# Optimization experiments

Hardware: AMD Instinct MI355X
Metric: run time of the kernel (lower is better)

## Reference

```python
import jax, jax.numpy as jnp
import numpy as np

V_SIZE = 128000  # vocab size (v_size init arg)


def setup_inputs() -> dict:
    key = jax.random.key(0)
    k1, k2 = jax.random.split(key)
    # per-position scores -> weighting_scheme (softmax over seq dim)
    w_es = jax.random.normal(k1, (256, 2048), dtype=jnp.float32)
    # instance['x']: token ids in [0, v_size)
    x = jax.random.randint(k2, (256, 2048), 0, V_SIZE, dtype=jnp.int64)
    return {"w_es": w_es, "x": x}


def reference(w_es, x):
    # weighting_scheme(indices, w_es, instance): softmax over sequence positions
    weights = jax.nn.softmax(w_es, axis=-1)          # [B, S]
    B, S = weights.shape
    rows = jnp.arange(B)[:, None]                    # [B, 1] broadcast against [B, S]
    # scatter: w_a[b, x[b, i]] = weights[b, i]  (vectorized index_put)
    w_a = jnp.zeros((B, V_SIZE), dtype=weights.dtype).at[rows, x].set(weights)
    return (w_a, weights)
```

## Files before the change

### kernel.cpp

```cpp
#include <hip/hip_runtime.h>

#define BATCH 256
#define SEQ   2048
#define VOCAB 128000
#define HALF   64000
#define PCHUNK 16000
#define NPH    4

typedef float v4f __attribute__((ext_vector_type(4)));
typedef int   v4i __attribute__((ext_vector_type(4)));
typedef float v2f __attribute__((ext_vector_type(2)));
typedef int   v2i __attribute__((ext_vector_type(2)));

#define LBAR() do { asm volatile("s_waitcnt lgkmcnt(0)" ::: "memory"); \
                    __builtin_amdgcn_s_barrier(); } while (0)

__global__ __launch_bounds__(1024, 4)
void softmax_scatter_phased(const float* __restrict__ w_es,
                            const int*   __restrict__ x,
                            float* __restrict__ w_a,
                            float* __restrict__ w_out)
{
    __shared__ int   chunk[PCHUNK];
    __shared__ float red[32];

    const int bid = blockIdx.x;
    const int r = bid & (BATCH - 1);
    const int h = bid >> 8;
    const int base0 = h * HALF;

    const int t = threadIdx.x;
    const int lane = t & 63;
    const int wid  = t >> 6;

    {
        const v4i m1 = (v4i)(-1);
        #pragma unroll
        for (int j0 = 0; j0 < 4096; j0 += 1024) {
            const int j = j0 + t;
            if (j < (PCHUNK >> 2)) ((v4i*)chunk)[j] = m1;
        }
    }

    const float* rowp = w_es + (size_t)r * SEQ;
    const v2f a = ((const v2f*)rowp)[t];

    float m = fmaxf(a.x, a.y);
    #pragma unroll
    for (int off = 32; off > 0; off >>= 1)
        m = fmaxf(m, __shfl_down(m, off, 64));
    if (lane == 0) red[wid] = m;
    __syncthreads();
    m = red[0];
    #pragma unroll
    for (int k = 1; k < 16; ++k) m = fmaxf(m, red[k]);

    const float e0 = __expf(a.x - m);
    const float e1 = __expf(a.y - m);
    float s = e0 + e1;
    #pragma unroll
    for (int off = 32; off > 0; off >>= 1)
        s += __shfl_down(s, off, 64);
    if (lane == 0) red[16 + wid] = s;
    __syncthreads();
    s = red[16];
    #pragma unroll
    for (int k = 1; k < 16; ++k) s += red[16 + k];

    const float inv = 1.0f / s;
    const float w0 = e0 * inv;
    const float w1 = e1 * inv;

    if (h == 0) {
        v2f wv; wv.x = w0; wv.y = w1;
        ((v2f*)(w_out + (size_t)r * SEQ))[t] = wv;
    }

    const v2i xv = ((const v2i*)(x + (size_t)r * SEQ))[t];
    const int i0 = 2 * t;
    const int i1 = 2 * t + 1;

    float* const growp = w_a + (size_t)r * VOCAB;

    for (int p = 0; p < NPH; ++p) {
        const int pb = base0 + p * PCHUNK;
        const int v0 = xv.x - pb;
        const int v1 = xv.y - pb;
        const bool in0 = (unsigned)v0 < (unsigned)PCHUNK;
        const bool in1 = (unsigned)v1 < (unsigned)PCHUNK;

        if (in0) atomicMax(&chunk[v0], i0);
        if (in1) atomicMax(&chunk[v1], i1);
        LBAR();

        if (in0 && chunk[v0] == i0) ((float*)chunk)[v0] = w0;
        if (in1 && chunk[v1] == i1) ((float*)chunk)[v1] = w1;
        LBAR();

        float* gp = growp + pb;
        #pragma unroll
        for (int j0 = 0; j0 < 4096; j0 += 1024) {
            const int j = j0 + t;
            if (j < (PCHUNK >> 2)) {
                v4i b = ((const v4i*)chunk)[j];
                v4f o;
                o.x = (b.x < 0) ? 0.0f : __int_as_float(b.x);
                o.y = (b.y < 0) ? 0.0f : __int_as_float(b.y);
                o.z = (b.z < 0) ? 0.0f : __int_as_float(b.z);
                o.w = (b.w < 0) ? 0.0f : __int_as_float(b.w);
                ((v4f*)gp)[j] = o;
            }
        }

        if (p < NPH - 1) {
            LBAR();
            const v4i m1 = (v4i)(-1);
            #pragma unroll
            for (int j0 = 0; j0 < 4096; j0 += 1024) {
                const int j = j0 + t;
                if (j < (PCHUNK >> 2)) ((v4i*)chunk)[j] = m1;
            }
            LBAR();
        }
    }
}

extern "C" void kernel_launch(void* const* d_in, const int* in_sizes, int n_in,
                              void* d_out, int out_size, void* d_ws, size_t ws_size,
                              hipStream_t stream) {
    const float* w_es = (const float*)d_in[0];
    const int*   x    = (const int*)d_in[1];

    float* out  = (float*)d_out;
    float* w_a  = out;
    float* w    = out + (size_t)BATCH * VOCAB;

    softmax_scatter_phased<<<2 * BATCH, 1024, 0, stream>>>(w_es, x, w_a, w);
}
```

Baseline: 136.6 us.

## Replace phased LDS chunk scatter with LDS hash table plus occupancy bitmap

Each block now inserts its in-range token ids into a 4096-slot open-addressing hash table in shared memory. The table resolves duplicate ids by atomicMax on the position, then swaps in the winning softmax weight. A bitmap marks occupied vocab entries, so the block writes its whole 64000-entry half of the output row in one pass, probing the hash only for set bits. This removes the four-phase loop with its repeated chunk clears and barriers, and shrinks LDS use, which may raise occupancy. In exchange it adds CAS-based linear probing and hash lookups during the write-out.

```diff
diff --git a/kernel.cpp b/kernel.cpp
--- a/kernel.cpp
+++ b/kernel.cpp
@@ -3,9 +3,8 @@
 #define BATCH 256
 #define SEQ   2048
 #define VOCAB 128000
-#define HALF   64000
-#define PCHUNK 16000
-#define NPH    4
+#define HALF  64000
+#define HSLOT 4096
 
 typedef float v4f __attribute__((ext_vector_type(4)));
 typedef int   v4i __attribute__((ext_vector_type(4)));
@@ -15,35 +14,37 @@
 #define LBAR() do { asm volatile("s_waitcnt lgkmcnt(0)" ::: "memory"); \
                     __builtin_amdgcn_s_barrier(); } while (0)
 
+__device__ __forceinline__ int hash_v(int v) {
+    return (int)(((unsigned)v * 2654435761u) >> 20);
+}
+
 __global__ __launch_bounds__(1024, 4)
-void softmax_scatter_phased(const float* __restrict__ w_es,
-                            const int*   __restrict__ x,
-                            float* __restrict__ w_a,
-                            float* __restrict__ w_out)
+void softmax_scatter_hash(const float* __restrict__ w_es,
+                          const int*   __restrict__ x,
+                          float* __restrict__ w_a,
+                          float* __restrict__ w_out)
 {
-    __shared__ int   chunk[PCHUNK];
-    __shared__ float red[32];
+    __shared__ int      key[HSLOT];
+    __shared__ int      val[HSLOT];
+    __shared__ unsigned bm[HALF / 32];
+    __shared__ float    red[32];
 
     const int bid = blockIdx.x;
     const int r = bid & (BATCH - 1);
     const int h = bid >> 8;
-    const int base0 = h * HALF;
-
     const int t = threadIdx.x;
     const int lane = t & 63;
     const int wid  = t >> 6;
 
     {
         const v4i m1 = (v4i)(-1);
-        #pragma unroll
-        for (int j0 = 0; j0 < 4096; j0 += 1024) {
-            const int j = j0 + t;
-            if (j < (PCHUNK >> 2)) ((v4i*)chunk)[j] = m1;
-        }
+        ((v4i*)key)[t] = m1;
+        ((v4i*)val)[t] = m1;
+        if (t < (HALF / 32 / 4)) ((v4i*)bm)[t] = (v4i)(0);
     }
 
-    const float* rowp = w_es + (size_t)r * SEQ;
-    const v2f a = ((const v2f*)rowp)[t];
+    const v2f a  = ((const v2f*)(w_es + (size_t)r * SEQ))[t];
+    const v2i xv = ((const v2i*)(x    + (size_t)r * SEQ))[t];
 
     float m = fmaxf(a.x, a.y);
     #pragma unroll
@@ -54,6 +55,34 @@
     m = red[0];
     #pragma unroll
     for (int k = 1; k < 16; ++k) m = fmaxf(m, red[k]);
+
+    const int i0 = 2 * t;
+    const int i1 = 2 * t + 1;
+    const int v0 = xv.x - h * HALF;
+    const int v1 = xv.y - h * HALF;
+    const bool in0 = (unsigned)v0 < (unsigned)HALF;
+    const bool in1 = (unsigned)v1 < (unsigned)HALF;
+
+    if (in0) {
+        atomicOr(&bm[v0 >> 5], 1u << (v0 & 31));
+        int s = hash_v(v0);
+        while (true) {
+            int k = atomicCAS(&key[s], -1, v0);
+            if (k == -1 || k == v0) break;
+            s = (s + 1) & (HSLOT - 1);
+        }
+        atomicMax(&val[s], i0);
+    }
+    if (in1) {
+        atomicOr(&bm[v1 >> 5], 1u << (v1 & 31));
+        int s = hash_v(v1);
+        while (true) {
+            int k = atomicCAS(&key[s], -1, v1);
+            if (k == -1 || k == v1) break;
+            s = (s + 1) & (HSLOT - 1);
+        }
+        atomicMax(&val[s], i1);
+    }
 
     const float e0 = __expf(a.x - m);
     const float e1 = __expf(a.y - m);
@@ -76,52 +105,35 @@
         ((v2f*)(w_out + (size_t)r * SEQ))[t] = wv;
     }
 
-    const v2i xv = ((const v2i*)(x + (size_t)r * SEQ))[t];
-    const int i0 = 2 * t;
-    const int i1 = 2 * t + 1;
+    if (in0) {
+        int sl = hash_v(v0);
+        while (key[sl] != v0) sl = (sl + 1) & (HSLOT - 1);
+        if (val[sl] == i0) val[sl] = __float_as_int(w0);
+    }
+    if (in1) {
+        int sl = hash_v(v1);
+        while (key[sl] != v1) sl = (sl + 1) & (HSLOT - 1);
+        if (val[sl] == i1) val[sl] = __float_as_int(w1);
+    }
+    LBAR();
 
-    float* const growp = w_a + (size_t)r * VOCAB;
-
-    for (int p = 0; p < NPH; ++p) {
-        const int pb = base0 + p * PCHUNK;
-        const int v0 = xv.x - pb;
-        const int v1 = xv.y - pb;
-        const bool in0 = (unsigned)v0 < (unsigned)PCHUNK;
-        const bool in1 = (unsigned)v1 < (unsigned)PCHUNK;
-
-        if (in0) atomicMax(&chunk[v0], i0);
-        if (in1) atomicMax(&chunk[v1], i1);
-        LBAR();
-
-        if (in0 && chunk[v0] == i0) ((float*)chunk)[v0] = w0;
-        if (in1 && chunk[v1] == i1) ((float*)chunk)[v1] = w1;
-        LBAR();
-
-        float* gp = growp + pb;
-        #pragma unroll
-        for (int j0 = 0; j0 < 4096; j0 += 1024) {
-            const int j = j0 + t;
-            if (j < (PCHUNK >> 2)) {
-                v4i b = ((const v4i*)chunk)[j];
-                v4f o;
-                o.x = (b.x < 0) ? 0.0f : __int_as_float(b.x);
-                o.y = (b.y < 0) ? 0.0f : __int_as_float(b.y);
-                o.z = (b.z < 0) ? 0.0f : __int_as_float(b.z);
-                o.w = (b.w < 0) ? 0.0f : __int_as_float(b.w);
-                ((v4f*)gp)[j] = o;
+    float* gp = w_a + (size_t)r * VOCAB + h * HALF;
+    for (int g = t; g < (HALF >> 2); g += 1024) {
+        const unsigned word = bm[g >> 3];
+        const unsigned nib  = (word >> ((g & 7) << 2)) & 0xFu;
+        v4f o = (v4f)(0.0f);
+        if (nib) {
+            #pragma unroll
+            for (int k = 0; k < 4; ++k) {
+                if (nib & (1u << k)) {
+                    const int v = (g << 2) + k;
+                    int sl = hash_v(v);
+                    while (key[sl] != v) sl = (sl + 1) & (HSLOT - 1);
+                    o[k] = __int_as_float(val[sl]);
+                }
             }
         }
-
-        if (p < NPH - 1) {
-            LBAR();
-            const v4i m1 = (v4i)(-1);
-            #pragma unroll
-            for (int j0 = 0; j0 < 4096; j0 += 1024) {
-                const int j = j0 + t;
-                if (j < (PCHUNK >> 2)) ((v4i*)chunk)[j] = m1;
-            }
-            LBAR();
-        }
+        ((v4f*)gp)[g] = o;
     }
 }
 
@@ -135,5 +147,5 @@
     float* w_a  = out;
     float* w    = out + (size_t)BATCH * VOCAB;
 
-    softmax_scatter_phased<<<2 * BATCH, 1024, 0, stream>>>(w_es, x, w_a, w);
+    softmax_scatter_hash<<<2 * BATCH, 1024, 0, stream>>>(w_es, x, w_a, w);
 }
```

Result: no change. 138.2 us (+1.2%).
